# Kernel tuning notes

Hardware: AMD Instinct MI355X
Metric: run time of the kernel (lower is better)

Reference implementation:

```python
import jax, jax.numpy as jnp
import numpy as np

E = 8          # num experts
TOPK = 2
D = 1024       # emb_size (expert hidden == emb_size)


def setup_inputs() -> dict:
    key = jax.random.key(0)
    ks = jax.random.split(key, 8)
    s = 1.0 / np.sqrt(D)
    x = jax.random.normal(ks[0], (4, 1024, D), dtype=jnp.float32)
    gate_W = jax.random.uniform(ks[1], (E, D), jnp.float32, -s, s)   # torch Linear weight (out,in)
    gate_b = jax.random.uniform(ks[2], (E,), jnp.float32, -s, s)
    w1 = jax.random.uniform(ks[3], (E, D, D), jnp.float32, -s, s)    # per-expert first Linear (out,in)
    b1 = jax.random.uniform(ks[4], (E, D), jnp.float32, -s, s)
    w2 = jax.random.uniform(ks[5], (E, D, D), jnp.float32, -s, s)    # per-expert second Linear (out,in)
    b2 = jax.random.uniform(ks[6], (E, D), jnp.float32, -s, s)
    return {"x": x, "gate_W": gate_W, "gate_b": gate_b,
            "w1": w1, "b1": b1, "w2": w2, "b2": b2}


def reference(x, gate_W, gate_b, w1, b1, w2, b2):
    x_shape = x.shape
    xt = x.reshape(-1, x_shape[-1])                       # [N, D]

    # gating
    gate_logits = xt @ gate_W.T + gate_b                  # [N, E]
    gate_prob = jax.nn.softmax(gate_logits, axis=-1)      # [N, E]
    top_w, top_i = jax.lax.top_k(gate_prob, TOPK)         # [N, K]
    top_w = jax.nn.softmax(top_w, axis=-1)                # renormalize over top-k

    # dense per-expert MLP: h = relu(x @ W1^T + b1); o = h @ W2^T + b2
    h = jax.nn.relu(jnp.einsum('nd,ehd->neh', xt, w1) + b1[None])   # [N, E, D]
    o = jnp.einsum('neh,eoh->neo', h, w2) + b2[None]                # [N, E, D]

    # gather top-k expert outputs per token and combine with weights
    o_top = jnp.take_along_axis(o, top_i[:, :, None], axis=1)       # [N, K, D]
    y = jnp.sum(o_top * top_w[:, :, None], axis=1)                  # [N, D]

    return y.reshape(x_shape), gate_prob
```

## Files before the change

kernel.cpp:

```cpp
#include <hip/hip_runtime.h>

#define NTOK 4096
#define DIM 1024
#define NE 8
#define NPAIR (NTOK * 2)
#define NSLOT 17

typedef __bf16 bf16x8 __attribute__((ext_vector_type(8)));
typedef float floatx4 __attribute__((ext_vector_type(4)));

__device__ __forceinline__ unsigned short f2bf(float f) {
  unsigned u = __float_as_uint(f);
  u = u + 0x7fffu + ((u >> 16) & 1u);
  return (unsigned short)(u >> 16);
}
__device__ __forceinline__ float bf2f(unsigned short h) {
  return __uint_as_float(((unsigned)h) << 16);
}

__device__ __forceinline__ void gld_lds16(const unsigned short* g, unsigned short* l) {
  __builtin_amdgcn_global_load_lds(
      (const __attribute__((address_space(1))) void*)g,
      (__attribute__((address_space(3))) void*)l, 16, 0, 0);
}

__global__ __launch_bounds__(256) void gate_kernel(
    const float* __restrict__ x, const float* __restrict__ gW,
    const float* __restrict__ gb,
    float* __restrict__ gp_out, int2* __restrict__ tops,
    float* __restrict__ pairw, int* __restrict__ cnt, int* __restrict__ done,
    unsigned short* __restrict__ x_bf)
{
  const int tid = threadIdx.x;
  if (blockIdx.x == 0) {
    if (tid < NE) cnt[tid] = 0;
    if (tid == NE) *done = 0;
  }
  const int lane = tid & 63;
  const int wid = tid >> 6;
  const int t = blockIdx.x * 4 + wid;

  float4 xv[4];
#pragma unroll
  for (int j = 0; j < 4; j++)
    xv[j] = ((const float4*)(x + (size_t)t * DIM))[lane + 64 * j];

#pragma unroll
  for (int j = 0; j < 4; j++) {
    ushort4 o;
    o.x = f2bf(xv[j].x); o.y = f2bf(xv[j].y);
    o.z = f2bf(xv[j].z); o.w = f2bf(xv[j].w);
    ((ushort4*)(x_bf + (size_t)t * DIM))[lane + 64 * j] = o;
  }

  float p[NE];
#pragma unroll
  for (int e = 0; e < NE; e++) {
    const float4* gwe = (const float4*)(gW + e * DIM);
    float s = 0.f;
#pragma unroll
    for (int j = 0; j < 4; j++) {
      float4 g = gwe[lane + 64 * j];
      s += xv[j].x * g.x + xv[j].y * g.y + xv[j].z * g.z + xv[j].w * g.w;
    }
    p[e] = s;
  }
#pragma unroll
  for (int e = 0; e < NE; e++) {
#pragma unroll
    for (int off = 32; off >= 1; off >>= 1) p[e] += __shfl_xor(p[e], off);
  }

  float m = -1e30f;
#pragma unroll
  for (int e = 0; e < NE; e++) { p[e] += gb[e]; m = fmaxf(m, p[e]); }
  float s = 0.f;
  float pr[NE];
#pragma unroll
  for (int e = 0; e < NE; e++) { pr[e] = __expf(p[e] - m); s += pr[e]; }
  float inv = 1.f / s;
#pragma unroll
  for (int e = 0; e < NE; e++) pr[e] *= inv;

  if (lane < NE) gp_out[(size_t)t * NE + lane] = pr[lane];

  if (lane == 0) {
    int i0 = 0;
#pragma unroll
    for (int e = 1; e < NE; e++) if (pr[e] > pr[i0]) i0 = e;
    int i1 = (i0 == 0) ? 1 : 0;
#pragma unroll
    for (int e = 0; e < NE; e++) if (e != i0 && pr[e] > pr[i1]) i1 = e;
    float d = __expf(pr[i1] - pr[i0]);
    float w0 = 1.f / (1.f + d);
    tops[t] = make_int2(i0, i1);
    pairw[t * 2] = w0;
    pairw[t * 2 + 1] = 1.f - w0;
  }
}

__global__ __launch_bounds__(256) void bin_sched_kernel(
    const int2* __restrict__ tops, int* __restrict__ cnt,
    int* __restrict__ bucket,
    int* __restrict__ posmap,
    int* __restrict__ done, int* __restrict__ base,
    int* __restrict__ sched, int* __restrict__ sched_n)
{
  const int t = blockIdx.x * 256 + threadIdx.x;
  const int lane = threadIdx.x & 63;
  int2 ti = tops[t];
#pragma unroll
  for (int slot = 0; slot < 2; slot++) {
    int e = slot ? ti.y : ti.x;
#pragma unroll
    for (int ex = 0; ex < NE; ex++) {
      bool mine = (e == ex);
      unsigned long long mask = __ballot(mine);
      if (mask) {
        int leader = __ffsll((long long)mask) - 1;
        int total = __popcll(mask);
        int prefix = __popcll(mask & ((1ull << lane) - 1ull));
        int idx = 0;
        if (lane == leader) idx = atomicAdd(&cnt[ex], total);
        idx = __shfl(idx, leader) + prefix;
        if (mine) {
          bucket[ex * NTOK + idx] = t * 2 + slot;
          posmap[t * 2 + slot] = (ex << 16) | idx;
        }
      }
    }
  }
  __syncthreads();
  if (threadIdx.x == 0) {
    if (atomicAdd(done, 1) == gridDim.x - 1) {
      int b = 0, pos = 0;
      for (int e = 0; e < NE; e++) {
        int c = atomicAdd(&cnt[e], 0);
        base[e] = b;
        int tiles = (c + 63) >> 6;
        for (int i = 0; i < tiles; i++) {
          int valid = c - i * 64; if (valid > 64) valid = 64;
          sched[pos++] = (e << 20) | (i << 8) | valid;
        }
        b += c;
      }
      base[NE] = b;
      *sched_n = pos;
    }
  }
}

__global__ __launch_bounds__(256) void cvt_kernel(
    const float4* __restrict__ src, ushort4* __restrict__ dst)
{
  const int i = blockIdx.x * 256 + threadIdx.x;
  float4 v = src[i];
  ushort4 o;
  o.x = f2bf(v.x); o.y = f2bf(v.y); o.z = f2bf(v.z); o.w = f2bf(v.w);
  dst[i] = o;
}

template <int RELU, int GATHER>
__global__ __launch_bounds__(256) void ffn_gemm(
    const unsigned short* __restrict__ A,
    const unsigned short* __restrict__ B,
    const float* __restrict__ bias,
    const int* __restrict__ base,
    const int* __restrict__ bucket,
    const int* __restrict__ sched, const int* __restrict__ sched_n,
    unsigned short* __restrict__ Out)
{
  const int l = blockIdx.x;
  const int xcd = l & 7;
  const int w = l >> 3;
  const int nt = w & 7;
  const int slot = xcd * NSLOT + (w >> 3);
  if (slot >= *sched_n) return;
  const int se = sched[slot];
  const int e = se >> 20;
  const int mt = (se >> 8) & 0xfff;
  const int valid = se & 255;
  const int arow0 = base[e] + mt * 64;

  __shared__ unsigned short lda[64 * 64];
  __shared__ unsigned short ldb[128 * 64];

  const int tid = threadIdx.x;
  const int lane = tid & 63;
  const int wid = tid >> 6;

  const unsigned short* ap[2];
  const unsigned short* bp[4];
#pragma unroll
  for (int j = 0; j < 2; j++) {
    int g = wid * 2 + j;
    int row = g * 8 + (lane >> 3);
    int gran = (lane & 7) ^ (row & 7);
    if (GATHER) {
      int idx = mt * 64 + row;
      int ce = base[e + 1] - base[e];
      if (idx > ce - 1) idx = ce - 1;
      int tok = bucket[e * NTOK + idx] >> 1;
      ap[j] = A + (size_t)tok * DIM + (gran << 3);
    } else {
      int prow = arow0 + row;
      if (prow > NPAIR - 1) prow = NPAIR - 1;
      ap[j] = A + (size_t)prow * DIM + (gran << 3);
    }
  }
#pragma unroll
  for (int j = 0; j < 4; j++) {
    int g = wid * 4 + j;
    int row = g * 8 + (lane >> 3);
    int gran = (lane & 7) ^ (row & 7);
    bp[j] = B + ((size_t)e * DIM + nt * 128 + row) * DIM + (gran << 3);
  }

  floatx4 acc[4][2] = {};
  const int wn = wid * 32;
  const int quad = lane >> 4;
  const int cl = lane & 15;
  const int sw = cl & 7;

  for (int k0 = 0; k0 < 16; k0++) {
#pragma unroll
    for (int j = 0; j < 2; j++) {
      gld_lds16(ap[j], &lda[(wid * 2 + j) * 512]);
      ap[j] += 64;
    }
#pragma unroll
    for (int j = 0; j < 4; j++) {
      gld_lds16(bp[j], &ldb[(wid * 4 + j) * 512]);
      bp[j] += 64;
    }
    __syncthreads();
#pragma unroll
    for (int kk = 0; kk < 64; kk += 32) {
      const int gb = (kk >> 3) + quad;
      const int goff = ((gb ^ sw) << 3);
      bf16x8 af[4], bfr[2];
#pragma unroll
      for (int mi = 0; mi < 4; mi++)
        af[mi] = *(const bf16x8*)&lda[(mi * 16 + cl) * 64 + goff];
#pragma unroll
      for (int ni = 0; ni < 2; ni++)
        bfr[ni] = *(const bf16x8*)&ldb[(wn + ni * 16 + cl) * 64 + goff];
#pragma unroll
      for (int mi = 0; mi < 4; mi++)
#pragma unroll
        for (int ni = 0; ni < 2; ni++)
          acc[mi][ni] = __builtin_amdgcn_mfma_f32_16x16x32_bf16(af[mi], bfr[ni], acc[mi][ni], 0, 0, 0);
    }
    if (k0 < 15) __syncthreads();
  }

#pragma unroll
  for (int ni = 0; ni < 2; ni++) {
    int col = nt * 128 + wn + ni * 16 + cl;
    float bval = bias[e * DIM + col];
#pragma unroll
    for (int mi = 0; mi < 4; mi++) {
#pragma unroll
      for (int reg = 0; reg < 4; reg++) {
        int rl = mi * 16 + quad * 4 + reg;
        if (rl < valid) {
          float v = acc[mi][ni][reg] + bval;
          if (RELU) v = fmaxf(v, 0.f);
          Out[(size_t)(arow0 + rl) * DIM + col] = f2bf(v);
        }
      }
    }
  }
}

__global__ __launch_bounds__(256) void combine_kernel(
    const unsigned short* __restrict__ o, const int* __restrict__ posmap,
    const int* __restrict__ base, const float* __restrict__ pairw,
    float* __restrict__ y)
{
  const int t = blockIdx.x;
  const int tid = threadIdx.x;
  const int pm0 = posmap[t * 2], pm1 = posmap[t * 2 + 1];
  const int p0 = base[pm0 >> 16] + (pm0 & 0xffff);
  const int p1 = base[pm1 >> 16] + (pm1 & 0xffff);
  const float w0 = pairw[t * 2], w1 = pairw[t * 2 + 1];
  ushort4 a = ((const ushort4*)(o + (size_t)p0 * DIM))[tid];
  ushort4 b = ((const ushort4*)(o + (size_t)p1 * DIM))[tid];
  float4 r;
  r.x = w0 * bf2f(a.x) + w1 * bf2f(b.x);
  r.y = w0 * bf2f(a.y) + w1 * bf2f(b.y);
  r.z = w0 * bf2f(a.z) + w1 * bf2f(b.z);
  r.w = w0 * bf2f(a.w) + w1 * bf2f(b.w);
  ((float4*)(y + (size_t)t * DIM))[tid] = r;
}

extern "C" void kernel_launch(void* const* d_in, const int* in_sizes, int n_in,
                              void* d_out, int out_size, void* d_ws, size_t ws_size,
                              hipStream_t stream) {
  const float* x  = (const float*)d_in[0];
  const float* gW = (const float*)d_in[1];
  const float* gb = (const float*)d_in[2];
  const float* w1 = (const float*)d_in[3];
  const float* b1 = (const float*)d_in[4];
  const float* w2 = (const float*)d_in[5];
  const float* b2 = (const float*)d_in[6];
  float* y  = (float*)d_out;
  float* gp = (float*)d_out + (size_t)NTOK * DIM;

  char* ws = (char*)d_ws;
  unsigned short* x_bf   = (unsigned short*)(ws);
  unsigned short* w2_bf  = (unsigned short*)(ws);
  unsigned short* h_pack = (unsigned short*)(ws + (size_t)(16u << 20));
  unsigned short* w1_bf  = (unsigned short*)(ws + (size_t)(32u << 20));
  unsigned short* o_pack = (unsigned short*)(ws + (size_t)(32u << 20));
  char* tail = ws + (size_t)(48u << 20);
  int*   cnt     = (int*)(tail);
  int*   done    = cnt + NE;
  int*   base    = done + 1;
  int*   sched   = base + NE + 1;
  int*   sched_n = sched + 256;
  int*   bucket  = sched_n + 1;
  float* pairw   = (float*)(bucket + NE * NTOK);
  int2*  tops    = (int2*)(pairw + NPAIR);
  int*   posmap  = (int*)(tops + NTOK);

  const int cvt_blocks = (NE * DIM * DIM / 4) / 256;
  const int gemm_grid = 8 * NSLOT * 8;
  gate_kernel<<<NTOK / 4, 256, 0, stream>>>(x, gW, gb, gp, tops, pairw, cnt, done, x_bf);
  bin_sched_kernel<<<NTOK / 256, 256, 0, stream>>>(tops, cnt, bucket, posmap, done,
                                                   base, sched, sched_n);
  cvt_kernel<<<cvt_blocks, 256, 0, stream>>>((const float4*)w1, (ushort4*)w1_bf);
  ffn_gemm<1, 1><<<gemm_grid, 256, 0, stream>>>(x_bf, w1_bf, b1, base, bucket, sched, sched_n, h_pack);
  cvt_kernel<<<cvt_blocks, 256, 0, stream>>>((const float4*)w2, (ushort4*)w2_bf);
  ffn_gemm<0, 0><<<gemm_grid, 256, 0, stream>>>(h_pack, w2_bf, b2, base, bucket, sched, sched_n, o_pack);
  combine_kernel<<<NTOK, 256, 0, stream>>>(o_pack, posmap, base, pairw, y);
}
```

Before: 233.5 us.

## Fuse gating with binning and enlarge expert GEMM tiles to 128x128

The binning step moves into the gate kernel: each token does per-expert atomics directly, which drops the separate bin kernel and the intermediate tops buffer. Counter reset moves into the first weight-convert kernel, which now launches before gating. The expert GEMM grows from 64x128 to 128x128 tiles with 512 threads (8 waves in a 2x4 layout), so weight tiles are re-read from memory about half as often, and the schedule is rebuilt for 128-row tiles. The trade-offs are fewer blocks in flight, more padding waste on partial tiles, and more contended scalar atomics in binning.

Result: slower. 323.0 us (+38.3%).

```diff
diff --git a/kernel.cpp b/kernel.cpp
--- a/kernel.cpp
+++ b/kernel.cpp
@@ -4,7 +4,6 @@
 #define DIM 1024
 #define NE 8
 #define NPAIR (NTOK * 2)
-#define NSLOT 17
 
 typedef __bf16 bf16x8 __attribute__((ext_vector_type(8)));
 typedef float floatx4 __attribute__((ext_vector_type(4)));
@@ -24,18 +23,18 @@
       (__attribute__((address_space(3))) void*)l, 16, 0, 0);
 }
 
-__global__ __launch_bounds__(256) void gate_kernel(
+__global__ __launch_bounds__(256) void gate_bin_kernel(
     const float* __restrict__ x, const float* __restrict__ gW,
     const float* __restrict__ gb,
-    float* __restrict__ gp_out, int2* __restrict__ tops,
-    float* __restrict__ pairw, int* __restrict__ cnt, int* __restrict__ done,
+    float* __restrict__ gp_out, float* __restrict__ pairw,
+    int* __restrict__ cnt, int* __restrict__ done,
+    int* __restrict__ bucket,
+    int* __restrict__ posmap,
+    int* __restrict__ base,
+    int* __restrict__ sched, int* __restrict__ sched_n,
     unsigned short* __restrict__ x_bf)
 {
   const int tid = threadIdx.x;
-  if (blockIdx.x == 0) {
-    if (tid < NE) cnt[tid] = 0;
-    if (tid == NE) *done = 0;
-  }
   const int lane = tid & 63;
   const int wid = tid >> 6;
   const int t = blockIdx.x * 4 + wid;
@@ -93,53 +92,26 @@
     for (int e = 0; e < NE; e++) if (e != i0 && pr[e] > pr[i1]) i1 = e;
     float d = __expf(pr[i1] - pr[i0]);
     float w0 = 1.f / (1.f + d);
-    tops[t] = make_int2(i0, i1);
     pairw[t * 2] = w0;
     pairw[t * 2 + 1] = 1.f - w0;
-  }
-}
-
-__global__ __launch_bounds__(256) void bin_sched_kernel(
-    const int2* __restrict__ tops, int* __restrict__ cnt,
-    int* __restrict__ bucket,
-    int* __restrict__ posmap,
-    int* __restrict__ done, int* __restrict__ base,
-    int* __restrict__ sched, int* __restrict__ sched_n)
-{
-  const int t = blockIdx.x * 256 + threadIdx.x;
-  const int lane = threadIdx.x & 63;
-  int2 ti = tops[t];
-#pragma unroll
-  for (int slot = 0; slot < 2; slot++) {
-    int e = slot ? ti.y : ti.x;
-#pragma unroll
-    for (int ex = 0; ex < NE; ex++) {
-      bool mine = (e == ex);
-      unsigned long long mask = __ballot(mine);
-      if (mask) {
-        int leader = __ffsll((long long)mask) - 1;
-        int total = __popcll(mask);
-        int prefix = __popcll(mask & ((1ull << lane) - 1ull));
-        int idx = 0;
-        if (lane == leader) idx = atomicAdd(&cnt[ex], total);
-        idx = __shfl(idx, leader) + prefix;
-        if (mine) {
-          bucket[ex * NTOK + idx] = t * 2 + slot;
-          posmap[t * 2 + slot] = (ex << 16) | idx;
-        }
-      }
-    }
+    int idx0 = atomicAdd(&cnt[i0], 1);
+    bucket[i0 * NTOK + idx0] = t * 2;
+    posmap[t * 2] = (i0 << 16) | idx0;
+    int idx1 = atomicAdd(&cnt[i1], 1);
+    bucket[i1 * NTOK + idx1] = t * 2 + 1;
+    posmap[t * 2 + 1] = (i1 << 16) | idx1;
   }
   __syncthreads();
-  if (threadIdx.x == 0) {
+  if (tid == 0) {
+    __threadfence();
     if (atomicAdd(done, 1) == gridDim.x - 1) {
       int b = 0, pos = 0;
       for (int e = 0; e < NE; e++) {
         int c = atomicAdd(&cnt[e], 0);
         base[e] = b;
-        int tiles = (c + 63) >> 6;
+        int tiles = (c + 127) >> 7;
         for (int i = 0; i < tiles; i++) {
-          int valid = c - i * 64; if (valid > 64) valid = 64;
+          int valid = c - i * 128; if (valid > 128) valid = 128;
           sched[pos++] = (e << 20) | (i << 8) | valid;
         }
         b += c;
@@ -151,8 +123,9 @@
 }
 
 __global__ __launch_bounds__(256) void cvt_kernel(
-    const float4* __restrict__ src, ushort4* __restrict__ dst)
+    const float4* __restrict__ src, ushort4* __restrict__ dst, int* cnt9)
 {
+  if (cnt9 && blockIdx.x == 0 && threadIdx.x < NE + 1) cnt9[threadIdx.x] = 0;
   const int i = blockIdx.x * 256 + threadIdx.x;
   float4 v = src[i];
   ushort4 o;
@@ -161,7 +134,7 @@
 }
 
 template <int RELU, int GATHER>
-__global__ __launch_bounds__(256) void ffn_gemm(
+__global__ __launch_bounds__(512) void ffn_gemm(
     const unsigned short* __restrict__ A,
     const unsigned short* __restrict__ B,
     const float* __restrict__ bias,
@@ -174,15 +147,15 @@
   const int xcd = l & 7;
   const int w = l >> 3;
   const int nt = w & 7;
-  const int slot = xcd * NSLOT + (w >> 3);
+  const int slot = xcd * 9 + (w >> 3);
   if (slot >= *sched_n) return;
   const int se = sched[slot];
   const int e = se >> 20;
   const int mt = (se >> 8) & 0xfff;
   const int valid = se & 255;
-  const int arow0 = base[e] + mt * 64;
-
-  __shared__ unsigned short lda[64 * 64];
+  const int arow0 = base[e] + mt * 128;
+
+  __shared__ unsigned short lda[128 * 64];
   __shared__ unsigned short ldb[128 * 64];
 
   const int tid = threadIdx.x;
@@ -190,14 +163,14 @@
   const int wid = tid >> 6;
 
   const unsigned short* ap[2];
-  const unsigned short* bp[4];
+  const unsigned short* bp[2];
 #pragma unroll
   for (int j = 0; j < 2; j++) {
     int g = wid * 2 + j;
     int row = g * 8 + (lane >> 3);
     int gran = (lane & 7) ^ (row & 7);
     if (GATHER) {
-      int idx = mt * 64 + row;
+      int idx = mt * 128 + row;
       int ce = base[e + 1] - base[e];
       if (idx > ce - 1) idx = ce - 1;
       int tok = bucket[e * NTOK + idx] >> 1;
@@ -207,17 +180,12 @@
       if (prow > NPAIR - 1) prow = NPAIR - 1;
       ap[j] = A + (size_t)prow * DIM + (gran << 3);
     }
-  }
-#pragma unroll
-  for (int j = 0; j < 4; j++) {
-    int g = wid * 4 + j;
-    int row = g * 8 + (lane >> 3);
-    int gran = (lane & 7) ^ (row & 7);
     bp[j] = B + ((size_t)e * DIM + nt * 128 + row) * DIM + (gran << 3);
   }
 
   floatx4 acc[4][2] = {};
-  const int wn = wid * 32;
+  const int wm = (wid & 1) * 64;
+  const int wn = (wid >> 1) * 32;
   const int quad = lane >> 4;
   const int cl = lane & 15;
   const int sw = cl & 7;
@@ -226,11 +194,8 @@
 #pragma unroll
     for (int j = 0; j < 2; j++) {
       gld_lds16(ap[j], &lda[(wid * 2 + j) * 512]);
+      gld_lds16(bp[j], &ldb[(wid * 2 + j) * 512]);
       ap[j] += 64;
-    }
-#pragma unroll
-    for (int j = 0; j < 4; j++) {
-      gld_lds16(bp[j], &ldb[(wid * 4 + j) * 512]);
       bp[j] += 64;
     }
     __syncthreads();
@@ -241,7 +206,7 @@
       bf16x8 af[4], bfr[2];
 #pragma unroll
       for (int mi = 0; mi < 4; mi++)
-        af[mi] = *(const bf16x8*)&lda[(mi * 16 + cl) * 64 + goff];
+        af[mi] = *(const bf16x8*)&lda[(wm + mi * 16 + cl) * 64 + goff];
 #pragma unroll
       for (int ni = 0; ni < 2; ni++)
         bfr[ni] = *(const bf16x8*)&ldb[(wn + ni * 16 + cl) * 64 + goff];
@@ -262,7 +227,7 @@
     for (int mi = 0; mi < 4; mi++) {
 #pragma unroll
       for (int reg = 0; reg < 4; reg++) {
-        int rl = mi * 16 + quad * 4 + reg;
+        int rl = wm + mi * 16 + quad * 4 + reg;
         if (rl < valid) {
           float v = acc[mi][ni][reg] + bval;
           if (RELU) v = fmaxf(v, 0.f);
@@ -321,17 +286,15 @@
   int*   sched_n = sched + 256;
   int*   bucket  = sched_n + 1;
   float* pairw   = (float*)(bucket + NE * NTOK);
-  int2*  tops    = (int2*)(pairw + NPAIR);
-  int*   posmap  = (int*)(tops + NTOK);
+  int*   posmap  = (int*)(pairw + NPAIR);
 
   const int cvt_blocks = (NE * DIM * DIM / 4) / 256;
-  const int gemm_grid = 8 * NSLOT * 8;
-  gate_kernel<<<NTOK / 4, 256, 0, stream>>>(x, gW, gb, gp, tops, pairw, cnt, done, x_bf);
-  bin_sched_kernel<<<NTOK / 256, 256, 0, stream>>>(tops, cnt, bucket, posmap, done,
-                                                   base, sched, sched_n);
-  cvt_kernel<<<cvt_blocks, 256, 0, stream>>>((const float4*)w1, (ushort4*)w1_bf);
-  ffn_gemm<1, 1><<<gemm_grid, 256, 0, stream>>>(x_bf, w1_bf, b1, base, bucket, sched, sched_n, h_pack);
-  cvt_kernel<<<cvt_blocks, 256, 0, stream>>>((const float4*)w2, (ushort4*)w2_bf);
-  ffn_gemm<0, 0><<<gemm_grid, 256, 0, stream>>>(h_pack, w2_bf, b2, base, bucket, sched, sched_n, o_pack);
+  const int gemm_grid = 576;
+  cvt_kernel<<<cvt_blocks, 256, 0, stream>>>((const float4*)w1, (ushort4*)w1_bf, cnt);
+  gate_bin_kernel<<<NTOK / 4, 256, 0, stream>>>(x, gW, gb, gp, pairw, cnt, done,
+                                                bucket, posmap, base, sched, sched_n, x_bf);
+  ffn_gemm<1, 1><<<gemm_grid, 512, 0, stream>>>(x_bf, w1_bf, b1, base, bucket, sched, sched_n, h_pack);
+  cvt_kernel<<<cvt_blocks, 256, 0, stream>>>((const float4*)w2, (ushort4*)w2_bf, nullptr);
+  ffn_gemm<0, 0><<<gemm_grid, 512, 0, stream>>>(h_pack, w2_bf, b2, base, bucket, sched, sched_n, o_pack);
   combine_kernel<<<NTOK, 256, 0, stream>>>(o_pack, posmap, base, pairw, y);
 }
```

## Double GEMM M-tile to 128 rows with 8 waves and merge weight conversions

Applied to the files above, without the earlier changes.

The expert GEMM now processes 128 token rows per block instead of 64, using 512 threads arranged as a 2x4 wave grid. Each B tile is therefore reused across twice as many rows, which halves B traffic and the number of scheduled tiles. The schedule and grid are shrunk to match. Both fp32-to-bf16 weight conversions now run as a single up-front launch, which required re-laying out the workspace so w2_bf no longer aliases x_bf. The cost is a larger padded tail per expert tile and fewer blocks to keep the GPU busy.

Result: faster. 222.0 us (-4.9%).

```diff
diff --git a/kernel.cpp b/kernel.cpp
--- a/kernel.cpp
+++ b/kernel.cpp
@@ -4,7 +4,6 @@
 #define DIM 1024
 #define NE 8
 #define NPAIR (NTOK * 2)
-#define NSLOT 17
 
 typedef __bf16 bf16x8 __attribute__((ext_vector_type(8)));
 typedef float floatx4 __attribute__((ext_vector_type(4)));
@@ -137,9 +136,9 @@
       for (int e = 0; e < NE; e++) {
         int c = atomicAdd(&cnt[e], 0);
         base[e] = b;
-        int tiles = (c + 63) >> 6;
+        int tiles = (c + 127) >> 7;
         for (int i = 0; i < tiles; i++) {
-          int valid = c - i * 64; if (valid > 64) valid = 64;
+          int valid = c - i * 128; if (valid > 128) valid = 128;
           sched[pos++] = (e << 20) | (i << 8) | valid;
         }
         b += c;
@@ -150,10 +149,15 @@
   }
 }
 
-__global__ __launch_bounds__(256) void cvt_kernel(
-    const float4* __restrict__ src, ushort4* __restrict__ dst)
-{
-  const int i = blockIdx.x * 256 + threadIdx.x;
+__global__ __launch_bounds__(256) void cvt2_kernel(
+    const float4* __restrict__ src1, ushort4* __restrict__ dst1,
+    const float4* __restrict__ src2, ushort4* __restrict__ dst2, int half_blocks)
+{
+  int b = blockIdx.x;
+  const float4* src = src1;
+  ushort4* dst = dst1;
+  if (b >= half_blocks) { b -= half_blocks; src = src2; dst = dst2; }
+  const int i = b * 256 + threadIdx.x;
   float4 v = src[i];
   ushort4 o;
   o.x = f2bf(v.x); o.y = f2bf(v.y); o.z = f2bf(v.z); o.w = f2bf(v.w);
@@ -161,7 +165,7 @@
 }
 
 template <int RELU, int GATHER>
-__global__ __launch_bounds__(256) void ffn_gemm(
+__global__ __launch_bounds__(512) void ffn_gemm(
     const unsigned short* __restrict__ A,
     const unsigned short* __restrict__ B,
     const float* __restrict__ bias,
@@ -174,15 +178,15 @@
   const int xcd = l & 7;
   const int w = l >> 3;
   const int nt = w & 7;
-  const int slot = xcd * NSLOT + (w >> 3);
+  const int slot = xcd * 9 + (w >> 3);
   if (slot >= *sched_n) return;
   const int se = sched[slot];
   const int e = se >> 20;
   const int mt = (se >> 8) & 0xfff;
   const int valid = se & 255;
-  const int arow0 = base[e] + mt * 64;
-
-  __shared__ unsigned short lda[64 * 64];
+  const int arow0 = base[e] + mt * 128;
+
+  __shared__ unsigned short lda[128 * 64];
   __shared__ unsigned short ldb[128 * 64];
 
   const int tid = threadIdx.x;
@@ -190,14 +194,14 @@
   const int wid = tid >> 6;
 
   const unsigned short* ap[2];
-  const unsigned short* bp[4];
+  const unsigned short* bp[2];
 #pragma unroll
   for (int j = 0; j < 2; j++) {
     int g = wid * 2 + j;
     int row = g * 8 + (lane >> 3);
     int gran = (lane & 7) ^ (row & 7);
     if (GATHER) {
-      int idx = mt * 64 + row;
+      int idx = mt * 128 + row;
       int ce = base[e + 1] - base[e];
       if (idx > ce - 1) idx = ce - 1;
       int tok = bucket[e * NTOK + idx] >> 1;
@@ -207,17 +211,12 @@
       if (prow > NPAIR - 1) prow = NPAIR - 1;
       ap[j] = A + (size_t)prow * DIM + (gran << 3);
     }
-  }
-#pragma unroll
-  for (int j = 0; j < 4; j++) {
-    int g = wid * 4 + j;
-    int row = g * 8 + (lane >> 3);
-    int gran = (lane & 7) ^ (row & 7);
     bp[j] = B + ((size_t)e * DIM + nt * 128 + row) * DIM + (gran << 3);
   }
 
   floatx4 acc[4][2] = {};
-  const int wn = wid * 32;
+  const int wm = (wid & 1) * 64;
+  const int wn = (wid >> 1) * 32;
   const int quad = lane >> 4;
   const int cl = lane & 15;
   const int sw = cl & 7;
@@ -226,11 +225,8 @@
 #pragma unroll
     for (int j = 0; j < 2; j++) {
       gld_lds16(ap[j], &lda[(wid * 2 + j) * 512]);
+      gld_lds16(bp[j], &ldb[(wid * 2 + j) * 512]);
       ap[j] += 64;
-    }
-#pragma unroll
-    for (int j = 0; j < 4; j++) {
-      gld_lds16(bp[j], &ldb[(wid * 4 + j) * 512]);
       bp[j] += 64;
     }
     __syncthreads();
@@ -241,7 +237,7 @@
       bf16x8 af[4], bfr[2];
 #pragma unroll
       for (int mi = 0; mi < 4; mi++)
-        af[mi] = *(const bf16x8*)&lda[(mi * 16 + cl) * 64 + goff];
+        af[mi] = *(const bf16x8*)&lda[(wm + mi * 16 + cl) * 64 + goff];
 #pragma unroll
       for (int ni = 0; ni < 2; ni++)
         bfr[ni] = *(const bf16x8*)&ldb[(wn + ni * 16 + cl) * 64 + goff];
@@ -262,7 +258,7 @@
     for (int mi = 0; mi < 4; mi++) {
 #pragma unroll
       for (int reg = 0; reg < 4; reg++) {
-        int rl = mi * 16 + quad * 4 + reg;
+        int rl = wm + mi * 16 + quad * 4 + reg;
         if (rl < valid) {
           float v = acc[mi][ni][reg] + bval;
           if (RELU) v = fmaxf(v, 0.f);
@@ -309,11 +305,11 @@
 
   char* ws = (char*)d_ws;
   unsigned short* x_bf   = (unsigned short*)(ws);
-  unsigned short* w2_bf  = (unsigned short*)(ws);
-  unsigned short* h_pack = (unsigned short*)(ws + (size_t)(16u << 20));
-  unsigned short* w1_bf  = (unsigned short*)(ws + (size_t)(32u << 20));
-  unsigned short* o_pack = (unsigned short*)(ws + (size_t)(32u << 20));
-  char* tail = ws + (size_t)(48u << 20);
+  unsigned short* w2_bf  = (unsigned short*)(ws + (size_t)(8u << 20));
+  unsigned short* h_pack = (unsigned short*)(ws + (size_t)(24u << 20));
+  unsigned short* w1_bf  = (unsigned short*)(ws + (size_t)(40u << 20));
+  unsigned short* o_pack = (unsigned short*)(ws + (size_t)(40u << 20));
+  char* tail = ws + (size_t)(56u << 20);
   int*   cnt     = (int*)(tail);
   int*   done    = cnt + NE;
   int*   base    = done + 1;
@@ -324,14 +320,14 @@
   int2*  tops    = (int2*)(pairw + NPAIR);
   int*   posmap  = (int*)(tops + NTOK);
 
-  const int cvt_blocks = (NE * DIM * DIM / 4) / 256;
-  const int gemm_grid = 8 * NSLOT * 8;
+  const int cvt_half = (NE * DIM * DIM / 4) / 256;
+  const int gemm_grid = 576;
+  cvt2_kernel<<<cvt_half * 2, 256, 0, stream>>>((const float4*)w1, (ushort4*)w1_bf,
+                                                (const float4*)w2, (ushort4*)w2_bf, cvt_half);
   gate_kernel<<<NTOK / 4, 256, 0, stream>>>(x, gW, gb, gp, tops, pairw, cnt, done, x_bf);
   bin_sched_kernel<<<NTOK / 256, 256, 0, stream>>>(tops, cnt, bucket, posmap, done,
                                                    base, sched, sched_n);
-  cvt_kernel<<<cvt_blocks, 256, 0, stream>>>((const float4*)w1, (ushort4*)w1_bf);
-  ffn_gemm<1, 1><<<gemm_grid, 256, 0, stream>>>(x_bf, w1_bf, b1, base, bucket, sched, sched_n, h_pack);
-  cvt_kernel<<<cvt_blocks, 256, 0, stream>>>((const float4*)w2, (ushort4*)w2_bf);
-  ffn_gemm<0, 0><<<gemm_grid, 256, 0, stream>>>(h_pack, w2_bf, b2, base, bucket, sched, sched_n, o_pack);
+  ffn_gemm<1, 1><<<gemm_grid, 512, 0, stream>>>(x_bf, w1_bf, b1, base, bucket, sched, sched_n, h_pack);
+  ffn_gemm<0, 0><<<gemm_grid, 512, 0, stream>>>(h_pack, w2_bf, b2, base, bucket, sched, sched_n, o_pack);
   combine_kernel<<<NTOK, 256, 0, stream>>>(o_pack, posmap, base, pairw, y);
 }
```
